# Kernel tuning notes

Hardware: AMD Instinct MI355X
Metric: run time of the kernel (lower is better)

Reference implementation:

```python
import jax, jax.numpy as jnp
import numpy as np

H = 4  # num_heads

def setup_inputs() -> dict:
    key = jax.random.key(0)
    ks = jax.random.split(key, 9)
    B, S, D = 8, 2048, 256
    x = jax.random.normal(ks[0], (B, S, D), dtype=jnp.float32)
    scale = 1.0 / np.sqrt(D)
    Wq = jax.random.normal(ks[1], (D, D), dtype=jnp.float32) * scale
    bq = jnp.zeros((D,), dtype=jnp.float32)
    Wk = jax.random.normal(ks[2], (D, D), dtype=jnp.float32) * scale
    bk = jnp.zeros((D,), dtype=jnp.float32)
    Wv = jax.random.normal(ks[3], (D, D), dtype=jnp.float32) * scale
    bv = jnp.zeros((D,), dtype=jnp.float32)
    Wo = jax.random.normal(ks[4], (D, D), dtype=jnp.float32) * scale
    bo = jnp.zeros((D,), dtype=jnp.float32)
    return {"x": x, "Wq": Wq, "bq": bq, "Wk": Wk, "bk": bk,
            "Wv": Wv, "bv": bv, "Wo": Wo, "bo": bo}

def reference(x, Wq, bq, Wk, bk, Wv, bv, Wo, bo):
    B, S, D = x.shape
    hd = D // H
    inv_scale = 1.0 / jnp.sqrt(jnp.asarray(hd, x.dtype))
    # projections: torch Linear is x @ W.T + b; weights here stored as (D, D) used as x @ W + b
    def split_heads(t):
        return t.reshape(B, S, H, hd).transpose(0, 2, 1, 3)  # [B,H,S,hd]
    Q = split_heads(x @ Wq + bq)
    K = split_heads(x @ Wk + bk)
    V = split_heads(x @ Wv + bv)
    scores = jnp.einsum('bhqd,bhkd->bhqk', Q, K) * inv_scale  # [B,H,S,S]
    attn = jax.nn.softmax(scores, axis=-1)
    # dropout is identity in eval mode
    ctx = jnp.einsum('bhqk,bhkd->bhqd', attn, V)
    ctx = ctx.transpose(0, 2, 1, 3).reshape(B, S, D)
    return ctx @ Wo + bo
```

## Files before the change

### kernel.cpp

```cpp
#include <hip/hip_runtime.h>


typedef unsigned short u16;
typedef __bf16 bf16x8 __attribute__((ext_vector_type(8)));
typedef float  f32x4  __attribute__((ext_vector_type(4)));
typedef unsigned int u32x4 __attribute__((ext_vector_type(4)));
typedef unsigned int u32x2 __attribute__((ext_vector_type(2)));

#define LOG2E   1.4426950408889634f
#define ATTN_SC (0.125f * LOG2E)
#define PSTR    2097152
#define WPSTR   32768
#define WZSTR   65536

__device__ __forceinline__ u16 f2b(float f) {
  unsigned u = __builtin_bit_cast(unsigned, f);
  u += 0x7FFFu + ((u >> 16) & 1u);
  return (u16)(u >> 16);
}
__device__ __forceinline__ float b2f(u16 b) {
  return __builtin_bit_cast(float, (unsigned)b << 16);
}
__device__ __forceinline__ unsigned pack_trunc(float a, float b) {
  return (__builtin_bit_cast(unsigned, a) >> 16) | (__builtin_bit_cast(unsigned, b) & 0xFFFF0000u);
}
__device__ __forceinline__ unsigned pack_rne(float a, float b) {
  return (unsigned)f2b(a) | ((unsigned)f2b(b) << 16);
}
__device__ __forceinline__ f32x4 mfma16(bf16x8 a, bf16x8 b, f32x4 c) {
  return __builtin_amdgcn_mfma_f32_16x16x32_bf16(a, b, c, 0, 0, 0);
}
__device__ __forceinline__ void cp16(const u16* g, u16* l) {
  __builtin_amdgcn_global_load_lds((const __attribute__((address_space(1))) void*)g,
                                   (__attribute__((address_space(3))) void*)l, 16, 0, 0);
}

template <typename T>
__global__ __launch_bounds__(256) void prep(const T* __restrict__ x,
                                            const T* __restrict__ W0, const T* __restrict__ W1,
                                            const T* __restrict__ W2, const T* __restrict__ W3,
                                            const T* __restrict__ b0, const T* __restrict__ b1,
                                            const T* __restrict__ b2, const T* __restrict__ b3,
                                            u16* __restrict__ xp, u16* __restrict__ WTp,
                                            float* __restrict__ biasf) {
  int bid = blockIdx.x;
  if (bid < 4096) {
    int i0 = (bid * 256 + threadIdx.x) * 4;
    int row = i0 >> 8, col = i0 & 255;
    int p = col >> 7, pc = col & 127;
    u16* o = xp + (size_t)p * PSTR + (size_t)row * 128 + pc;
#pragma unroll
    for (int j = 0; j < 4; ++j) {
      if constexpr (sizeof(T) == 4) o[j] = f2b((float)x[i0 + j]);
      else                          o[j] = (u16)x[i0 + j];
    }
  } else {
    bid -= 4096;
    const int z = bid >> 8;
    const T* W = z == 0 ? W0 : z == 1 ? W1 : z == 2 ? W2 : W3;
    const T* b = z == 0 ? b0 : z == 1 ? b1 : z == 2 ? b2 : b3;
    int idx = (bid & 255) * 256 + threadIdx.x;
    int k = idx >> 8, n = idx & 255;
    u16 wb;
    if constexpr (sizeof(T) == 4) wb = f2b((float)W[k * 256 + n]);
    else                          wb = (u16)W[k * 256 + n];
    WTp[z * WZSTR + (k >> 7) * WPSTR + n * 128 + (k & 127)] = wb;
    if (idx < 256) {
      float bv;
      if constexpr (sizeof(T) == 4) bv = (float)b[idx];
      else                          bv = b2f((u16)b[idx]);
      biasf[z * 256 + idx] = bv;
    }
  }
}

__global__ __launch_bounds__(256, 2) void qkv_gemm(const u16* __restrict__ xp, const u16* __restrict__ WTp,
                                                   const float* __restrict__ biasf,
                                                   u16* __restrict__ Qw, u16* __restrict__ Kw,
                                                   u16* __restrict__ VTg) {
  __shared__ __align__(16) u16 Al[256 * 128];
  __shared__ __align__(16) u16 Bl[64 * 128];
  const int tid = threadIdx.x, w = tid >> 6, lane = tid & 63;
  const int l16 = lane & 15, quad = lane >> 4;
  const int z = blockIdx.z, n0 = blockIdx.y * 64, m0 = blockIdx.x * 256;
  const u16* Ab = xp + (size_t)m0 * 128;
  const u16* Bb = WTp + z * WZSTR + (size_t)n0 * 128;
  f32x4 acc[4][4];
#pragma unroll
  for (int mm = 0; mm < 4; ++mm)
#pragma unroll
    for (int nb = 0; nb < 4; ++nb) acc[mm][nb] = (f32x4){0.f, 0.f, 0.f, 0.f};

#pragma unroll
  for (int p = 0; p < 2; ++p) {
    __syncthreads();
    const u16* Ap = Ab + (size_t)p * PSTR;
    const u16* Bp = Bb + p * WPSTR;
#pragma unroll
    for (int i = 0; i < 16; ++i) {
      int slot = i * 256 + w * 64 + lane;
      int row = slot >> 4, pc = slot & 15, c = pc ^ (row & 15);
      cp16(Ap + (size_t)row * 128 + c * 8, Al + (i * 256 + w * 64) * 8);
    }
#pragma unroll
    for (int i = 0; i < 4; ++i) {
      int slot = i * 256 + w * 64 + lane;
      int row = slot >> 4, pc = slot & 15, c = pc ^ (row & 15);
      cp16(Bp + (size_t)row * 128 + c * 8, Bl + (i * 256 + w * 64) * 8);
    }
    __syncthreads();
#pragma unroll
    for (int kc = 0; kc < 4; ++kc) {
      int ch = ((kc * 4 + quad) ^ l16) * 8;
      bf16x8 a[4], b[4];
#pragma unroll
      for (int mm = 0; mm < 4; ++mm)
        a[mm] = *(const bf16x8*)&Al[(w * 64 + mm * 16 + l16) * 128 + ch];
#pragma unroll
      for (int nb = 0; nb < 4; ++nb)
        b[nb] = *(const bf16x8*)&Bl[(nb * 16 + l16) * 128 + ch];
#pragma unroll
      for (int mm = 0; mm < 4; ++mm)
#pragma unroll
        for (int nb = 0; nb < 4; ++nb)
          acc[mm][nb] = mfma16(a[mm], b[nb], acc[mm][nb]);
    }
  }

  const float* bp = biasf + z * 256;
  const int bb = m0 >> 11, s0 = m0 & 2047, h = blockIdx.y;
  if (z < 2) {
    u16* dst = (z == 0) ? Qw : Kw;
    const float sc = (z == 0) ? ATTN_SC : 1.0f;
#pragma unroll
    for (int mm = 0; mm < 4; ++mm)
#pragma unroll
      for (int nb = 0; nb < 4; ++nb) {
        int d = nb * 16 + l16;
        float bv = bp[n0 + d];
#pragma unroll
        for (int r = 0; r < 4; ++r) {
          int s = s0 + w * 64 + mm * 16 + quad * 4 + r;
          dst[(((size_t)(bb * 4 + h) * 2048) + s) * 64 + d] = f2b((acc[mm][nb][r] + bv) * sc);
        }
      }
  } else {
    __syncthreads();
#pragma unroll
    for (int mm = 0; mm < 4; ++mm)
#pragma unroll
      for (int nb = 0; nb < 4; ++nb) {
        int d = nb * 16 + l16;
        float bv = bp[n0 + d];
        f32x4 v = acc[mm][nb];
        u32x2 dd = { pack_rne(v[0] + bv, v[1] + bv), pack_rne(v[2] + bv, v[3] + bv) };
        int cch = w * 8 + mm * 2 + (quad >> 1);
        *(u32x2*)&Al[d * 256 + ((cch ^ (d & 31))) * 8 + (quad & 1) * 4] = dd;
      }
    __syncthreads();
#pragma unroll
    for (int i = 0; i < 8; ++i) {
      int slot = i * 256 + tid;
      int d = slot >> 5, pc = slot & 31;
      u32x4 vv = *(const u32x4*)&Al[d * 256 + ((pc ^ (d & 31))) * 8];
      *(u32x4*)(VTg + (((size_t)(bb * 4 + h) * 64) + d) * 2048 + s0 + pc * 8) = vv;
    }
  }
}

template <bool OUT_BF16>
__global__ __launch_bounds__(256) void out_gemm(const u16* __restrict__ ctxp, const u16* __restrict__ WTp,
                                                const float* __restrict__ bo, void* __restrict__ outv) {
  __shared__ __align__(16) u16 Al[128 * 128];
  __shared__ __align__(16) u16 Bl[64 * 128];
  const int tid = threadIdx.x, w = tid >> 6, lane = tid & 63;
  const int l16 = lane & 15, quad = lane >> 4;
  const int n0 = blockIdx.y * 64, m0 = blockIdx.x * 128;
  const u16* Ab = ctxp + (size_t)m0 * 128;
  const u16* Bb = WTp + 3 * WZSTR + (size_t)n0 * 128;
  f32x4 acc[2][4];
#pragma unroll
  for (int mm = 0; mm < 2; ++mm)
#pragma unroll
    for (int nb = 0; nb < 4; ++nb) acc[mm][nb] = (f32x4){0.f, 0.f, 0.f, 0.f};

#pragma unroll
  for (int p = 0; p < 2; ++p) {
    __syncthreads();
    const u16* Ap = Ab + (size_t)p * PSTR;
    const u16* Bp = Bb + p * WPSTR;
#pragma unroll
    for (int i = 0; i < 8; ++i) {
      int slot = i * 256 + w * 64 + lane;
      int row = slot >> 4, pc = slot & 15, c = pc ^ (row & 15);
      cp16(Ap + (size_t)row * 128 + c * 8, Al + (i * 256 + w * 64) * 8);
    }
#pragma unroll
    for (int i = 0; i < 4; ++i) {
      int slot = i * 256 + w * 64 + lane;
      int row = slot >> 4, pc = slot & 15, c = pc ^ (row & 15);
      cp16(Bp + (size_t)row * 128 + c * 8, Bl + (i * 256 + w * 64) * 8);
    }
    __syncthreads();
#pragma unroll
    for (int kc = 0; kc < 4; ++kc) {
      int ch = ((kc * 4 + quad) ^ l16) * 8;
      bf16x8 a0 = *(const bf16x8*)&Al[(w * 32 + l16) * 128 + ch];
      bf16x8 a1 = *(const bf16x8*)&Al[(w * 32 + 16 + l16) * 128 + ch];
#pragma unroll
      for (int nb = 0; nb < 4; ++nb) {
        bf16x8 b = *(const bf16x8*)&Bl[(nb * 16 + l16) * 128 + ch];
        acc[0][nb] = mfma16(a0, b, acc[0][nb]);
        acc[1][nb] = mfma16(a1, b, acc[1][nb]);
      }
    }
  }
#pragma unroll
  for (int mm = 0; mm < 2; ++mm)
#pragma unroll
    for (int nb = 0; nb < 4; ++nb) {
      int n = n0 + nb * 16 + l16;
      float bv = bo[n];
#pragma unroll
      for (int r = 0; r < 4; ++r) {
        size_t m = m0 + w * 32 + mm * 16 + quad * 4 + r;
        float v = acc[mm][nb][r] + bv;
        if constexpr (OUT_BF16) ((u16*)outv)[m * 256 + n] = f2b(v);
        else                    ((float*)outv)[m * 256 + n] = v;
      }
    }
}

__global__ __launch_bounds__(128, 2) void attn(const u16* __restrict__ Q, const u16* __restrict__ K,
                                               const u16* __restrict__ VT, u16* __restrict__ ctxp) {
  __shared__ __align__(16) u16 Kt[2][64 * 64];
  __shared__ __align__(16) u16 VTt[2][64 * 64];
  __shared__ __align__(16) u16 Pt[2][2][16 * 64];
  const int tid = threadIdx.x;
  const int w = tid >> 6, lane = tid & 63;
  const int l16 = lane & 15, quad = lane >> 4;
  const int bh = blockIdx.y, q0 = blockIdx.x * 64;
  const u16* Qp = Q + (size_t)bh * 2048 * 64;
  const u16* Kp = K + (size_t)bh * 2048 * 64;
  const u16* Vp = VT + (size_t)bh * 64 * 2048;

  bf16x8 qf[2][2];
#pragma unroll
  for (int g = 0; g < 2; ++g) {
    int qrow = q0 + w * 32 + g * 16 + l16;
    qf[g][0] = *(const bf16x8*)(Qp + (size_t)qrow * 64 + quad * 8);
    qf[g][1] = *(const bf16x8*)(Qp + (size_t)qrow * 64 + 32 + quad * 8);
  }

  f32x4 acc[2][4];
#pragma unroll
  for (int g = 0; g < 2; ++g)
#pragma unroll
    for (int nb = 0; nb < 4; ++nb) acc[g][nb] = (f32x4){0.f, 0.f, 0.f, 0.f};
  float dn[2] = {0.f, 0.f};

  int srow[4], scol[4];
#pragma unroll
  for (int i = 0; i < 4; ++i) {
    int slot = i * 128 + tid;
    srow[i] = slot >> 3;
    scol[i] = (slot & 7) ^ (srow[i] & 7);
  }

#define STAGE(kt_, buf_)                                                                   \
  do {                                                                                     \
    _Pragma("unroll")                                                                      \
    for (int i = 0; i < 4; ++i) {                                                          \
      cp16(Kp + (size_t)((kt_) * 64 + srow[i]) * 64 + scol[i] * 8,                         \
           &Kt[buf_][(i * 128 + w * 64) * 8]);                                             \
      cp16(Vp + (size_t)srow[i] * 2048 + (kt_) * 64 + scol[i] * 8,                         \
           &VTt[buf_][(i * 128 + w * 64) * 8]);                                            \
    }                                                                                      \
  } while (0)

  STAGE(0, 0);

  for (int kt = 0; kt < 32; ++kt) {
    const int buf = kt & 1;
    __builtin_amdgcn_s_waitcnt(0x0F70 );
    __asm__ __volatile__("" ::: "memory");
    __builtin_amdgcn_s_barrier();
    __asm__ __volatile__("" ::: "memory");
    if (kt < 31) STAGE(kt + 1, buf ^ 1);

    const u16* KtB = Kt[buf];
    const u16* VtB = VTt[buf];

    bf16x8 vbr[2][4];
#pragma unroll
    for (int m = 0; m < 2; ++m)
#pragma unroll
      for (int nbD = 0; nbD < 4; ++nbD)
        vbr[m][nbD] = *(const bf16x8*)&VtB[(nbD * 16 + l16) * 64 + (((m * 4 + quad) ^ (l16 & 7))) * 8];

    f32x4 st[2][4];
#pragma unroll
    for (int g = 0; g < 2; ++g)
#pragma unroll
      for (int nb = 0; nb < 4; ++nb) st[g][nb] = (f32x4){0.f, 0.f, 0.f, 0.f};
#pragma unroll
    for (int kc = 0; kc < 2; ++kc) {
#pragma unroll
      for (int nbK = 0; nbK < 4; ++nbK) {
        bf16x8 a = *(const bf16x8*)&KtB[(nbK * 16 + l16) * 64 + (((kc * 4 + quad) ^ (l16 & 7))) * 8];
        st[0][nbK] = mfma16(a, qf[0][kc], st[0][nbK]);
        st[1][nbK] = mfma16(a, qf[1][kc], st[1][nbK]);
      }
    }

#pragma unroll
    for (int g = 0; g < 2; ++g) {
      u16* Ptg = Pt[w][g];
#pragma unroll
      for (int nbK = 0; nbK < 4; ++nbK) {
        float p0 = exp2f(st[g][nbK][0]), p1 = exp2f(st[g][nbK][1]);
        float p2 = exp2f(st[g][nbK][2]), p3 = exp2f(st[g][nbK][3]);
        dn[g] += (p0 + p1) + (p2 + p3);
        u32x2 dd = { pack_trunc(p0, p1), pack_trunc(p2, p3) };
        int cch = nbK * 2 + (quad >> 1);
        *(u32x2*)&Ptg[l16 * 64 + ((cch ^ (l16 & 7))) * 8 + (quad & 1) * 4] = dd;
      }
    }

#pragma unroll
    for (int m = 0; m < 2; ++m) {
#pragma unroll
      for (int g = 0; g < 2; ++g) {
        bf16x8 pb = *(const bf16x8*)&Pt[w][g][l16 * 64 + (((m * 4 + quad) ^ (l16 & 7))) * 8];
#pragma unroll
        for (int nbD = 0; nbD < 4; ++nbD)
          acc[g][nbD] = mfma16(vbr[m][nbD], pb, acc[g][nbD]);
      }
    }
  }
#undef STAGE

  float linv[2];
#pragma unroll
  for (int g = 0; g < 2; ++g) {
    float d = dn[g];
    d += __shfl_xor(d, 16);
    d += __shfl_xor(d, 32);
    linv[g] = 1.0f / d;
  }

#pragma unroll
  for (int g = 0; g < 2; ++g) {
    u16* Ptg = Pt[w][g];
#pragma unroll
    for (int nbD = 0; nbD < 4; ++nbD) {
      f32x4 v = acc[g][nbD];
      u32x2 dd = { pack_rne(v[0] * linv[g], v[1] * linv[g]),
                   pack_rne(v[2] * linv[g], v[3] * linv[g]) };
      int cch = nbD * 2 + (quad >> 1);
      *(u32x2*)&Ptg[l16 * 64 + ((cch ^ (l16 & 7))) * 8 + (quad & 1) * 4] = dd;
    }
  }
  const int bb = bh >> 2, h = bh & 3;
  const int p = h >> 1, pcol = (h & 1) * 64;
#pragma unroll
  for (int cc = 0; cc < 4; ++cc) {
    int slot = cc * 64 + lane;
    int row = slot >> 3, pc = slot & 7;
    u32x4 vv = *(const u32x4*)&Pt[w][0][row * 64 + ((pc ^ (row & 7))) * 8];
    size_t m = (size_t)bb * 2048 + q0 + w * 32 + row;
    *(u32x4*)&ctxp[(size_t)p * PSTR + m * 128 + pcol + pc * 8] = vv;
  }
}

extern "C" void kernel_launch(void* const* d_in, const int* in_sizes, int n_in,
                              void* d_out, int out_size, void* d_ws, size_t ws_size,
                              hipStream_t stream) {
  bool f32in = true;
  {
    void* basep = nullptr; size_t sz = 0;
    hipError_t e = hipMemGetAddressRange((hipDeviceptr_t*)&basep, &sz, (hipDeviceptr_t)d_in[0]);
    if (e == hipSuccess && sz > 0) f32in = sz >= (size_t)in_sizes[0] * 4;
    else f32in = false;
  }

  char* ws = (char*)d_ws;
  u16*   xp    = (u16*)(ws + 0);
  u16*   ctxp  = xp;
  u16*   WTp   = (u16*)(ws + 8388608);
  float* biasf = (float*)(ws + 8912896);
  u16*   Qw    = (u16*)(ws + 8916992);
  u16*   Kw    = (u16*)(ws + 17305600);
  u16*   VTg   = (u16*)(ws + 25694208);

  if (f32in) {
    prep<float><<<5120, 256, 0, stream>>>(
        (const float*)d_in[0],
        (const float*)d_in[1], (const float*)d_in[3], (const float*)d_in[5], (const float*)d_in[7],
        (const float*)d_in[2], (const float*)d_in[4], (const float*)d_in[6], (const float*)d_in[8],
        xp, WTp, biasf);
  } else {
    prep<u16><<<5120, 256, 0, stream>>>(
        (const u16*)d_in[0],
        (const u16*)d_in[1], (const u16*)d_in[3], (const u16*)d_in[5], (const u16*)d_in[7],
        (const u16*)d_in[2], (const u16*)d_in[4], (const u16*)d_in[6], (const u16*)d_in[8],
        xp, WTp, biasf);
  }
  qkv_gemm<<<dim3(64, 4, 3), 256, 0, stream>>>(xp, WTp, biasf, Qw, Kw, VTg);
  attn<<<dim3(32, 32), 128, 0, stream>>>(Qw, Kw, VTg, ctxp);
  if (f32in) out_gemm<false><<<dim3(128, 4), 256, 0, stream>>>(ctxp, WTp, biasf + 3 * 256, d_out);
  else       out_gemm<true ><<<dim3(128, 4), 256, 0, stream>>>(ctxp, WTp, biasf + 3 * 256, d_out);
}
```

Baseline: 174.1 us.

## Split attention over key halves and merge partial outputs in a combine kernel

The attention kernel now splits the key sequence into two halves via blockIdx.z. Each block uses 256 threads and covers 128 queries, and it writes unnormalized bf16 partial contexts plus softmax denominators. A new combine kernel sums the two partials, normalizes them and scatters the result into the packed context layout for the output GEMM. This is meant to raise parallelism and occupancy, at the cost of an extra launch, extra global traffic, and bf16 rounding of the partials before they are summed. It relies on the softmax having no running max (fixed-scale exp), so partials can be added directly.

Measured after the change: 173.6 us. No clear change (-0.3%).

```diff
diff --git a/kernel.cpp b/kernel.cpp
--- a/kernel.cpp
+++ b/kernel.cpp
@@ -20,6 +20,12 @@
 }
 __device__ __forceinline__ float b2f(u16 b) {
   return __builtin_bit_cast(float, (unsigned)b << 16);
+}
+__device__ __forceinline__ float b2f_hi(unsigned u) {
+  return __builtin_bit_cast(float, u & 0xFFFF0000u);
+}
+__device__ __forceinline__ float b2f_lo(unsigned u) {
+  return __builtin_bit_cast(float, u << 16);
 }
 __device__ __forceinline__ unsigned pack_trunc(float a, float b) {
   return (__builtin_bit_cast(unsigned, a) >> 16) | (__builtin_bit_cast(unsigned, b) & 0xFFFF0000u);
@@ -231,18 +237,20 @@
     }
 }
 
-__global__ __launch_bounds__(128, 2) void attn(const u16* __restrict__ Q, const u16* __restrict__ K,
-                                               const u16* __restrict__ VT, u16* __restrict__ ctxp) {
+__global__ __launch_bounds__(256, 3) void attn(const u16* __restrict__ Q, const u16* __restrict__ K,
+                                               const u16* __restrict__ VT,
+                                               u16* __restrict__ P0, u16* __restrict__ P1,
+                                               float* __restrict__ dnb) {
   __shared__ __align__(16) u16 Kt[2][64 * 64];
   __shared__ __align__(16) u16 VTt[2][64 * 64];
-  __shared__ __align__(16) u16 Pt[2][2][16 * 64];
+  __shared__ __align__(16) u16 Pt[4][2][16 * 64];
   const int tid = threadIdx.x;
   const int w = tid >> 6, lane = tid & 63;
   const int l16 = lane & 15, quad = lane >> 4;
-  const int bh = blockIdx.y, q0 = blockIdx.x * 64;
+  const int bh = blockIdx.y, q0 = blockIdx.x * 128, z = blockIdx.z;
   const u16* Qp = Q + (size_t)bh * 2048 * 64;
-  const u16* Kp = K + (size_t)bh * 2048 * 64;
-  const u16* Vp = VT + (size_t)bh * 64 * 2048;
+  const u16* Kp = K + (size_t)bh * 2048 * 64 + (size_t)z * 1024 * 64;
+  const u16* Vp = VT + (size_t)bh * 64 * 2048 + z * 1024;
 
   bf16x8 qf[2][2];
 #pragma unroll
@@ -259,34 +267,27 @@
     for (int nb = 0; nb < 4; ++nb) acc[g][nb] = (f32x4){0.f, 0.f, 0.f, 0.f};
   float dn[2] = {0.f, 0.f};
 
-  int srow[4], scol[4];
-#pragma unroll
-  for (int i = 0; i < 4; ++i) {
-    int slot = i * 128 + tid;
-    srow[i] = slot >> 3;
-    scol[i] = (slot & 7) ^ (srow[i] & 7);
-  }
+  const int sl0 = tid, sl1 = 256 + tid;
+  const int r0 = sl0 >> 3, c0 = (sl0 & 7) ^ (r0 & 7);
+  const int r1 = sl1 >> 3, c1 = (sl1 & 7) ^ (r1 & 7);
 
 #define STAGE(kt_, buf_)                                                                   \
   do {                                                                                     \
-    _Pragma("unroll")                                                                      \
-    for (int i = 0; i < 4; ++i) {                                                          \
-      cp16(Kp + (size_t)((kt_) * 64 + srow[i]) * 64 + scol[i] * 8,                         \
-           &Kt[buf_][(i * 128 + w * 64) * 8]);                                             \
-      cp16(Vp + (size_t)srow[i] * 2048 + (kt_) * 64 + scol[i] * 8,                         \
-           &VTt[buf_][(i * 128 + w * 64) * 8]);                                            \
-    }                                                                                      \
+    cp16(Kp + (size_t)((kt_) * 64 + r0) * 64 + c0 * 8, &Kt[buf_][(w * 64) * 8]);           \
+    cp16(Kp + (size_t)((kt_) * 64 + r1) * 64 + c1 * 8, &Kt[buf_][(256 + w * 64) * 8]);     \
+    cp16(Vp + (size_t)r0 * 2048 + (kt_) * 64 + c0 * 8, &VTt[buf_][(w * 64) * 8]);          \
+    cp16(Vp + (size_t)r1 * 2048 + (kt_) * 64 + c1 * 8, &VTt[buf_][(256 + w * 64) * 8]);    \
   } while (0)
 
   STAGE(0, 0);
 
-  for (int kt = 0; kt < 32; ++kt) {
+  for (int kt = 0; kt < 16; ++kt) {
     const int buf = kt & 1;
     __builtin_amdgcn_s_waitcnt(0x0F70 );
     __asm__ __volatile__("" ::: "memory");
     __builtin_amdgcn_s_barrier();
     __asm__ __volatile__("" ::: "memory");
-    if (kt < 31) STAGE(kt + 1, buf ^ 1);
+    if (kt < 15) STAGE(kt + 1, buf ^ 1);
 
     const u16* KtB = Kt[buf];
     const u16* VtB = VTt[buf];
@@ -340,13 +341,15 @@
   }
 #undef STAGE
 
-  float linv[2];
+  u16* pdst = z ? P1 : P0;
 #pragma unroll
   for (int g = 0; g < 2; ++g) {
     float d = dn[g];
     d += __shfl_xor(d, 16);
     d += __shfl_xor(d, 32);
-    linv[g] = 1.0f / d;
+    dn[g] = d;
+    if (quad == 0)
+      dnb[z * 65536 + bh * 2048 + q0 + w * 32 + g * 16 + l16] = d;
   }
 
 #pragma unroll
@@ -355,22 +358,39 @@
 #pragma unroll
     for (int nbD = 0; nbD < 4; ++nbD) {
       f32x4 v = acc[g][nbD];
-      u32x2 dd = { pack_rne(v[0] * linv[g], v[1] * linv[g]),
-                   pack_rne(v[2] * linv[g], v[3] * linv[g]) };
+      u32x2 dd = { pack_rne(v[0], v[1]), pack_rne(v[2], v[3]) };
       int cch = nbD * 2 + (quad >> 1);
       *(u32x2*)&Ptg[l16 * 64 + ((cch ^ (l16 & 7))) * 8 + (quad & 1) * 4] = dd;
     }
   }
-  const int bb = bh >> 2, h = bh & 3;
-  const int p = h >> 1, pcol = (h & 1) * 64;
 #pragma unroll
   for (int cc = 0; cc < 4; ++cc) {
     int slot = cc * 64 + lane;
     int row = slot >> 3, pc = slot & 7;
     u32x4 vv = *(const u32x4*)&Pt[w][0][row * 64 + ((pc ^ (row & 7))) * 8];
-    size_t m = (size_t)bb * 2048 + q0 + w * 32 + row;
-    *(u32x4*)&ctxp[(size_t)p * PSTR + m * 128 + pcol + pc * 8] = vv;
-  }
+    size_t qg = q0 + w * 32 + row;
+    *(u32x4*)(pdst + (((size_t)bh * 2048) + qg) * 64 + pc * 8) = vv;
+  }
+}
+
+__global__ __launch_bounds__(256) void combine(const u16* __restrict__ p0, const u16* __restrict__ p1,
+                                               const float* __restrict__ dnb, u16* __restrict__ ctxp) {
+  int t = blockIdx.x * 256 + threadIdx.x;
+  int chunk = t & 7, q = (t >> 3) & 2047, bh = t >> 14;
+  size_t idx = ((((size_t)bh * 2048) + q) * 64) + chunk * 8;
+  u32x4 a = *(const u32x4*)(p0 + idx);
+  u32x4 b = *(const u32x4*)(p1 + idx);
+  float l = 1.0f / (dnb[bh * 2048 + q] + dnb[65536 + bh * 2048 + q]);
+  u32x4 o;
+#pragma unroll
+  for (int i = 0; i < 4; ++i) {
+    float lo = (b2f_lo(a[i]) + b2f_lo(b[i])) * l;
+    float hi = (b2f_hi(a[i]) + b2f_hi(b[i])) * l;
+    o[i] = pack_rne(lo, hi);
+  }
+  int bb = bh >> 2, h = bh & 3, p = h >> 1, pcol = (h & 1) * 64;
+  size_t m = (size_t)bb * 2048 + q;
+  *(u32x4*)(ctxp + (size_t)p * PSTR + m * 128 + pcol + chunk * 8) = o;
 }
 
 extern "C" void kernel_launch(void* const* d_in, const int* in_sizes, int n_in,
@@ -386,12 +406,15 @@
 
   char* ws = (char*)d_ws;
   u16*   xp    = (u16*)(ws + 0);
-  u16*   ctxp  = xp;
   u16*   WTp   = (u16*)(ws + 8388608);
   float* biasf = (float*)(ws + 8912896);
   u16*   Qw    = (u16*)(ws + 8916992);
   u16*   Kw    = (u16*)(ws + 17305600);
   u16*   VTg   = (u16*)(ws + 25694208);
+  float* dnb   = (float*)(ws + 34082816);
+  u16*   part0 = xp;
+  u16*   part1 = (u16*)d_out;
+  u16*   ctxp  = Qw;
 
   if (f32in) {
     prep<float><<<5120, 256, 0, stream>>>(
@@ -407,7 +430,8 @@
         xp, WTp, biasf);
   }
   qkv_gemm<<<dim3(64, 4, 3), 256, 0, stream>>>(xp, WTp, biasf, Qw, Kw, VTg);
-  attn<<<dim3(32, 32), 128, 0, stream>>>(Qw, Kw, VTg, ctxp);
+  attn<<<dim3(16, 32, 2), 256, 0, stream>>>(Qw, Kw, VTg, part0, part1, dnb);
+  combine<<<2048, 256, 0, stream>>>(part0, part1, dnb, ctxp);
   if (f32in) out_gemm<false><<<dim3(128, 4), 256, 0, stream>>>(ctxp, WTp, biasf + 3 * 256, d_out);
   else       out_gemm<true ><<<dim3(128, 4), 256, 0, stream>>>(ctxp, WTp, biasf + 3 * 256, d_out);
 }
```
